# Kernel tuning notes

Measured on AMD Instinct MI355X. Metric: run time of the kernel, lower is better.

The kernel has to match this reference:

```python
import jax, jax.numpy as jnp
import numpy as np

H = 128  # hidden_size
I = 28   # input_size
C = 10   # num_classes


def setup_inputs() -> dict:
    key = jax.random.key(0)
    ks = jax.random.split(key, 11)
    s = 1.0 / np.sqrt(H)  # torch nn.RNN init scale
    return {
        "x": jax.random.normal(ks[0], (8192, 28, I), dtype=jnp.float32),
        "W_ih0": jax.random.uniform(ks[1], (H, I), jnp.float32, -s, s),
        "W_hh0": jax.random.uniform(ks[2], (H, H), jnp.float32, -s, s),
        "b_ih0": jax.random.uniform(ks[3], (H,), jnp.float32, -s, s),
        "b_hh0": jax.random.uniform(ks[4], (H,), jnp.float32, -s, s),
        "W_ih1": jax.random.uniform(ks[5], (H, H), jnp.float32, -s, s),
        "W_hh1": jax.random.uniform(ks[6], (H, H), jnp.float32, -s, s),
        "b_ih1": jax.random.uniform(ks[7], (H,), jnp.float32, -s, s),
        "b_hh1": jax.random.uniform(ks[8], (H,), jnp.float32, -s, s),
        "fc_w": jax.random.uniform(ks[9], (C, H), jnp.float32, -s, s),
        "fc_b": jax.random.uniform(ks[10], (C,), jnp.float32, -s, s),
    }


def _rnn_layer_full(x, W_ih, b_ih, W_hh, b_hh):
    # x: [B, T, D] -> full output sequence [B, T, H]
    B = x.shape[0]
    h0 = jnp.zeros((B, H), x.dtype)
    xw = jnp.einsum('btd,hd->bth', x, W_ih) + b_ih  # precompute input GEMM

    def step(h, xw_t):
        h = jnp.tanh(xw_t + h @ W_hh.T + b_hh)
        return h, h

    _, ys = jax.lax.scan(step, h0, jnp.swapaxes(xw, 0, 1))  # [T, B, H]
    return jnp.swapaxes(ys, 0, 1)


def _rnn_layer_last(x, W_ih, b_ih, W_hh, b_hh):
    # only the final hidden state is needed downstream
    B = x.shape[0]
    h0 = jnp.zeros((B, H), x.dtype)
    xw = jnp.einsum('btd,hd->bth', x, W_ih) + b_ih

    def step(h, xw_t):
        h = jnp.tanh(xw_t + h @ W_hh.T + b_hh)
        return h, None

    h_last, _ = jax.lax.scan(step, h0, jnp.swapaxes(xw, 0, 1))
    return h_last


def reference(x, W_ih0, W_hh0, b_ih0, b_hh0, W_ih1, W_hh1, b_ih1, b_hh1, fc_w, fc_b):
    out0 = _rnn_layer_full(x, W_ih0, b_ih0, W_hh0, b_hh0)   # [B, T, H]
    h_last = _rnn_layer_last(out0, W_ih1, b_ih1, W_hh1, b_hh1)  # [B, H] == out[:, -1, :]
    return h_last @ fc_w.T + fc_b  # [B, C]
```

## Files before the change

### kernel.cpp

```cpp
#include <hip/hip_runtime.h>

#define HSZ 128
#define ISZ 28
#define TSZ 28
#define CSZ 10
#define BT  16
#define NT  256
#define HBUF 2048

typedef _Float16 half_t;
typedef _Float16 v8h __attribute__((ext_vector_type(8)));
typedef _Float16 v4h __attribute__((ext_vector_type(4)));
typedef float v4f __attribute__((ext_vector_type(4)));

__device__ __forceinline__ float fast_tanh(float x) {
    float e = __expf(2.f * x);
    return 1.f - 2.f * __builtin_amdgcn_rcpf(e + 1.f);
}

__global__ __launch_bounds__(NT, 2)
void rnn_mfma6(const float* __restrict__ x,
               const float* __restrict__ W_ih0, const float* __restrict__ W_hh0,
               const float* __restrict__ b_ih0, const float* __restrict__ b_hh0,
               const float* __restrict__ W_ih1, const float* __restrict__ W_hh1,
               const float* __restrict__ b_ih1, const float* __restrict__ b_hh1,
               const float* __restrict__ fc_w, const float* __restrict__ fc_b,
               float* __restrict__ out)
{
    __shared__ half_t h0s[2][HBUF];
    __shared__ half_t h1s[2][HBUF];
    __shared__ half_t xs[TSZ][512];

    const int tid  = threadIdx.x;
    const int wave = tid >> 6;
    const int lane = tid & 63;
    const int ln   = lane & 15;
    const int quad = lane >> 4;
    const int b0   = blockIdx.x * BT;
    const int wbase = wave * 32;

    v8h aWx[2], aW0[2][4], aW1i[2][4], aW1h[2][4];
    v4f bias0[2], bias1[2];
#pragma unroll
    for (int rt = 0; rt < 2; ++rt) {
        const int row = wbase + rt * 16 + ln;
        {
            float4 p = *(const float4*)(b_ih0 + wbase + rt * 16 + quad * 4);
            float4 q = *(const float4*)(b_hh0 + wbase + rt * 16 + quad * 4);
            bias0[rt] = (v4f){p.x + q.x, p.y + q.y, p.z + q.z, p.w + q.w};
            p = *(const float4*)(b_ih1 + wbase + rt * 16 + quad * 4);
            q = *(const float4*)(b_hh1 + wbase + rt * 16 + quad * 4);
            bias1[rt] = (v4f){p.x + q.x, p.y + q.y, p.z + q.z, p.w + q.w};
        }
        {
            const float* pw = W_ih0 + row * ISZ + quad * 8;
            float4 a = *(const float4*)pw;
            float4 b = (quad < 3) ? *(const float4*)(pw + 4) : make_float4(0.f, 0.f, 0.f, 0.f);
            aWx[rt] = (v8h){(half_t)a.x, (half_t)a.y, (half_t)a.z, (half_t)a.w,
                            (half_t)b.x, (half_t)b.y, (half_t)b.z, (half_t)b.w};
        }
#pragma unroll
        for (int ks = 0; ks < 4; ++ks) {
            const float4* p0 = (const float4*)(W_hh0 + row * HSZ + ks * 32 + quad * 8);
            const float4* p1 = (const float4*)(W_ih1 + row * HSZ + ks * 32 + quad * 8);
            const float4* p2 = (const float4*)(W_hh1 + row * HSZ + ks * 32 + quad * 8);
            float4 a = p0[0], b = p0[1];
            aW0[rt][ks] = (v8h){(half_t)a.x, (half_t)a.y, (half_t)a.z, (half_t)a.w,
                                (half_t)b.x, (half_t)b.y, (half_t)b.z, (half_t)b.w};
            a = p1[0]; b = p1[1];
            aW1i[rt][ks] = (v8h){(half_t)a.x, (half_t)a.y, (half_t)a.z, (half_t)a.w,
                                 (half_t)b.x, (half_t)b.y, (half_t)b.z, (half_t)b.w};
            a = p2[0]; b = p2[1];
            aW1h[rt][ks] = (v8h){(half_t)a.x, (half_t)a.y, (half_t)a.z, (half_t)a.w,
                                 (half_t)b.x, (half_t)b.y, (half_t)b.z, (half_t)b.w};
        }
    }

    {
#pragma unroll
        for (int it = 0; it < 7; ++it) {
            const int c = tid + it * NT;
            const int q = c & 3;
            const int n = (c >> 2) & 15;
            const int t = c >> 6;
            const float* g = x + ((size_t)(b0 + n) * TSZ + t) * ISZ + q * 8;
            float4 a = *(const float4*)g;
            float4 b = (q < 3) ? *(const float4*)(g + 4) : make_float4(0.f, 0.f, 0.f, 0.f);
            v8h p = {(half_t)a.x, (half_t)a.y, (half_t)a.z, (half_t)a.w,
                     (half_t)b.x, (half_t)b.y, (half_t)b.z, (half_t)b.w};
            *(v8h*)&xs[t][(q * 16 + n) * 8] = p;
        }
    }

    *(v8h*)&h1s[0][tid * 8] = (v8h){(half_t)0.f, (half_t)0.f, (half_t)0.f, (half_t)0.f,
                                    (half_t)0.f, (half_t)0.f, (half_t)0.f, (half_t)0.f};
    __syncthreads();

    const int ws0 = wave * 512 + (quad >> 1) * 128 + ln * 8 + (quad & 1) * 4;
    const int ws1 = ws0 + 256;
    const int ro = lane * 8;

    {
        const v8h bx = *(const v8h*)&xs[0][ro];
#pragma unroll
        for (int rt = 0; rt < 2; ++rt) {
            v4f c = bias0[rt];
            c = __builtin_amdgcn_mfma_f32_16x16x32_f16(aWx[rt], bx, c, 0, 0, 0);
            v4h p = {(half_t)fast_tanh(c[0]), (half_t)fast_tanh(c[1]),
                     (half_t)fast_tanh(c[2]), (half_t)fast_tanh(c[3])};
            *(v4h*)&h0s[0][rt ? ws1 : ws0] = p;
        }
    }
    __syncthreads();

#pragma unroll 2
    for (int t = 0; t < TSZ - 1; ++t) {
        const int pr = t & 1;

        v8h bh0[4], bh1[4];
#pragma unroll
        for (int ks = 0; ks < 4; ++ks)
            bh0[ks] = *(const v8h*)&h0s[pr][ks * 512 + ro];
        const v8h bx = *(const v8h*)&xs[t + 1][ro];
#pragma unroll
        for (int ks = 0; ks < 4; ++ks)
            bh1[ks] = *(const v8h*)&h1s[pr][ks * 512 + ro];

#pragma unroll
        for (int rt = 0; rt < 2; ++rt) {
            v4f c = bias0[rt];
            c = __builtin_amdgcn_mfma_f32_16x16x32_f16(aWx[rt], bx, c, 0, 0, 0);
#pragma unroll
            for (int ks = 0; ks < 4; ++ks)
                c = __builtin_amdgcn_mfma_f32_16x16x32_f16(aW0[rt][ks], bh0[ks], c, 0, 0, 0);
            v4h p = {(half_t)fast_tanh(c[0]), (half_t)fast_tanh(c[1]),
                     (half_t)fast_tanh(c[2]), (half_t)fast_tanh(c[3])};
            *(v4h*)&h0s[pr ^ 1][rt ? ws1 : ws0] = p;
        }

#pragma unroll
        for (int rt = 0; rt < 2; ++rt) {
            v4f si = bias1[rt];
            v4f sh = (v4f){0.f, 0.f, 0.f, 0.f};
#pragma unroll
            for (int ks = 0; ks < 4; ++ks) {
                si = __builtin_amdgcn_mfma_f32_16x16x32_f16(aW1i[rt][ks], bh0[ks], si, 0, 0, 0);
                sh = __builtin_amdgcn_mfma_f32_16x16x32_f16(aW1h[rt][ks], bh1[ks], sh, 0, 0, 0);
            }
            const v4f a1 = si + sh;
            v4h p = {(half_t)fast_tanh(a1[0]), (half_t)fast_tanh(a1[1]),
                     (half_t)fast_tanh(a1[2]), (half_t)fast_tanh(a1[3])};
            *(v4h*)&h1s[pr ^ 1][rt ? ws1 : ws0] = p;
        }

        __syncthreads();
    }

    {
        const int pr = (TSZ - 1) & 1;
        v8h bh0[4], bh1[4];
#pragma unroll
        for (int ks = 0; ks < 4; ++ks) {
            bh0[ks] = *(const v8h*)&h0s[pr][ks * 512 + ro];
            bh1[ks] = *(const v8h*)&h1s[pr][ks * 512 + ro];
        }
#pragma unroll
        for (int rt = 0; rt < 2; ++rt) {
            v4f si = bias1[rt];
            v4f sh = (v4f){0.f, 0.f, 0.f, 0.f};
#pragma unroll
            for (int ks = 0; ks < 4; ++ks) {
                si = __builtin_amdgcn_mfma_f32_16x16x32_f16(aW1i[rt][ks], bh0[ks], si, 0, 0, 0);
                sh = __builtin_amdgcn_mfma_f32_16x16x32_f16(aW1h[rt][ks], bh1[ks], sh, 0, 0, 0);
            }
            const v4f a1 = si + sh;
            v4h p = {(half_t)fast_tanh(a1[0]), (half_t)fast_tanh(a1[1]),
                     (half_t)fast_tanh(a1[2]), (half_t)fast_tanh(a1[3])};
            *(v4h*)&h1s[pr ^ 1][rt ? ws1 : ws0] = p;
        }
    }
    __syncthreads();

    if (tid < BT * CSZ) {
        const int m = tid / CSZ, cc = tid - m * CSZ;
        float s = fc_b[cc];
#pragma unroll
        for (int ks = 0; ks < 4; ++ks) {
#pragma unroll
            for (int q2 = 0; q2 < 4; ++q2) {
                const v8h hv = *(const v8h*)&h1s[0][(ks * 64 + q2 * 16 + m) * 8];
                const int kb = ks * 32 + q2 * 8;
                const float4 w0 = *(const float4*)(fc_w + cc * HSZ + kb);
                const float4 w1 = *(const float4*)(fc_w + cc * HSZ + kb + 4);
                s += (float)hv[0] * w0.x + (float)hv[1] * w0.y +
                     (float)hv[2] * w0.z + (float)hv[3] * w0.w +
                     (float)hv[4] * w1.x + (float)hv[5] * w1.y +
                     (float)hv[6] * w1.z + (float)hv[7] * w1.w;
            }
        }
        out[(b0 + m) * CSZ + cc] = s;
    }
}

extern "C" void kernel_launch(void* const* d_in, const int* in_sizes, int n_in,
                              void* d_out, int out_size, void* d_ws, size_t ws_size,
                              hipStream_t stream) {
    const float* x     = (const float*)d_in[0];
    const float* W_ih0 = (const float*)d_in[1];
    const float* W_hh0 = (const float*)d_in[2];
    const float* b_ih0 = (const float*)d_in[3];
    const float* b_hh0 = (const float*)d_in[4];
    const float* W_ih1 = (const float*)d_in[5];
    const float* W_hh1 = (const float*)d_in[6];
    const float* b_ih1 = (const float*)d_in[7];
    const float* b_hh1 = (const float*)d_in[8];
    const float* fc_w  = (const float*)d_in[9];
    const float* fc_b  = (const float*)d_in[10];
    float* out = (float*)d_out;

    const int B = in_sizes[0] / (TSZ * ISZ);
    dim3 grid(B / BT), block(NT);
    rnn_mfma6<<<grid, block, 0, stream>>>(x, W_ih0, W_hh0, b_ih0, b_hh0,
                                          W_ih1, W_hh1, b_ih1, b_hh1,
                                          fc_w, fc_b, out);
}
```

Measured before the change: 128.1 us.

## Split layers into producer/consumer wave groups with flag-based ring-buffer sync

Four waves now run only the layer-0 recurrence and four waves run only the layer-1 recurrence. They hand hidden states through a 4-slot LDS ring and signal progress with per-wave volatile flags in shared memory, replacing the per-step block barrier. Each block now handles 32 sequences in two groups of 16 with 512 threads. This lets layer 0 run up to three steps ahead of layer 1, so the two layers overlap and register pressure per wave drops. It adds spin-wait polling on LDS and relies on LDS memory-ordering assumptions (waitcnt before the flag write) for correctness.

```diff
diff --git a/kernel.cpp b/kernel.cpp
--- a/kernel.cpp
+++ b/kernel.cpp
@@ -4,9 +4,9 @@
 #define ISZ 28
 #define TSZ 28
 #define CSZ 10
-#define BT  16
-#define NT  256
-#define HBUF 2048
+#define BT  32
+#define NG  2
+#define NT  512
 
 typedef _Float16 half_t;
 typedef _Float16 v8h __attribute__((ext_vector_type(8)));
@@ -18,18 +18,21 @@
     return 1.f - 2.f * __builtin_amdgcn_rcpf(e + 1.f);
 }
 
+__device__ __forceinline__ int imin(int a, int b) { return a < b ? a : b; }
+
 __global__ __launch_bounds__(NT, 2)
-void rnn_mfma6(const float* __restrict__ x,
-               const float* __restrict__ W_ih0, const float* __restrict__ W_hh0,
-               const float* __restrict__ b_ih0, const float* __restrict__ b_hh0,
-               const float* __restrict__ W_ih1, const float* __restrict__ W_hh1,
-               const float* __restrict__ b_ih1, const float* __restrict__ b_hh1,
-               const float* __restrict__ fc_w, const float* __restrict__ fc_b,
-               float* __restrict__ out)
+void rnn_pc(const float* __restrict__ x,
+            const float* __restrict__ W_ih0, const float* __restrict__ W_hh0,
+            const float* __restrict__ b_ih0, const float* __restrict__ b_hh0,
+            const float* __restrict__ W_ih1, const float* __restrict__ W_hh1,
+            const float* __restrict__ b_ih1, const float* __restrict__ b_hh1,
+            const float* __restrict__ fc_w, const float* __restrict__ fc_b,
+            float* __restrict__ out)
 {
-    __shared__ half_t h0s[2][HBUF];
-    __shared__ half_t h1s[2][HBUF];
-    __shared__ half_t xs[TSZ][512];
+    __shared__ half_t h0r[4][NG][2048];
+    __shared__ half_t h1r[4][NG][2048];
+    __shared__ half_t xs[TSZ][NG][512];
+    __shared__ int    flags[8];
 
     const int tid  = threadIdx.x;
     const int wave = tid >> 6;
@@ -37,158 +40,157 @@
     const int ln   = lane & 15;
     const int quad = lane >> 4;
     const int b0   = blockIdx.x * BT;
-    const int wbase = wave * 32;
-
-    v8h aWx[2], aW0[2][4], aW1i[2][4], aW1h[2][4];
-    v4f bias0[2], bias1[2];
-#pragma unroll
-    for (int rt = 0; rt < 2; ++rt) {
-        const int row = wbase + rt * 16 + ln;
-        {
-            float4 p = *(const float4*)(b_ih0 + wbase + rt * 16 + quad * 4);
-            float4 q = *(const float4*)(b_hh0 + wbase + rt * 16 + quad * 4);
+    const int w4   = wave & 3;
+    const int wsl  = w4 * 512 + (quad >> 1) * 128 + ln * 8 + (quad & 1) * 4;
+    const int ro   = lane * 8;
+    volatile int* vf = (volatile int*)flags;
+
+    {
+#pragma unroll
+        for (int it = 0; it < 7; ++it) {
+            const int c = tid + it * NT;
+            const int q = c & 3;
+            const int n = (c >> 2) & 15;
+            const int g = (c >> 6) & 1;
+            const int t = c >> 7;
+            const float* gp = x + ((size_t)(b0 + g * 16 + n) * TSZ + t) * ISZ + q * 8;
+            float4 a = *(const float4*)gp;
+            float4 b = (q < 3) ? *(const float4*)(gp + 4) : make_float4(0.f, 0.f, 0.f, 0.f);
+            v8h p = {(half_t)a.x, (half_t)a.y, (half_t)a.z, (half_t)a.w,
+                     (half_t)b.x, (half_t)b.y, (half_t)b.z, (half_t)b.w};
+            *(v8h*)&xs[t][g][(q * 16 + n) * 8] = p;
+        }
+    }
+    {
+        const v8h z = {(half_t)0.f, (half_t)0.f, (half_t)0.f, (half_t)0.f,
+                       (half_t)0.f, (half_t)0.f, (half_t)0.f, (half_t)0.f};
+        *(v8h*)&h0r[3][0][tid * 8] = z;
+        *(v8h*)&h1r[3][0][tid * 8] = z;
+        if (tid < 8) flags[tid] = 0;
+    }
+    __syncthreads();
+
+    if (wave < 4) {
+        v8h aWx[2], aW0[2][4];
+        v4f bias0[2];
+#pragma unroll
+        for (int rt = 0; rt < 2; ++rt) {
+            const int row = w4 * 32 + rt * 16 + ln;
+            float4 p = *(const float4*)(b_ih0 + w4 * 32 + rt * 16 + quad * 4);
+            float4 q = *(const float4*)(b_hh0 + w4 * 32 + rt * 16 + quad * 4);
             bias0[rt] = (v4f){p.x + q.x, p.y + q.y, p.z + q.z, p.w + q.w};
-            p = *(const float4*)(b_ih1 + wbase + rt * 16 + quad * 4);
-            q = *(const float4*)(b_hh1 + wbase + rt * 16 + quad * 4);
-            bias1[rt] = (v4f){p.x + q.x, p.y + q.y, p.z + q.z, p.w + q.w};
-        }
-        {
             const float* pw = W_ih0 + row * ISZ + quad * 8;
             float4 a = *(const float4*)pw;
             float4 b = (quad < 3) ? *(const float4*)(pw + 4) : make_float4(0.f, 0.f, 0.f, 0.f);
             aWx[rt] = (v8h){(half_t)a.x, (half_t)a.y, (half_t)a.z, (half_t)a.w,
                             (half_t)b.x, (half_t)b.y, (half_t)b.z, (half_t)b.w};
-        }
-#pragma unroll
-        for (int ks = 0; ks < 4; ++ks) {
-            const float4* p0 = (const float4*)(W_hh0 + row * HSZ + ks * 32 + quad * 8);
-            const float4* p1 = (const float4*)(W_ih1 + row * HSZ + ks * 32 + quad * 8);
-            const float4* p2 = (const float4*)(W_hh1 + row * HSZ + ks * 32 + quad * 8);
-            float4 a = p0[0], b = p0[1];
-            aW0[rt][ks] = (v8h){(half_t)a.x, (half_t)a.y, (half_t)a.z, (half_t)a.w,
-                                (half_t)b.x, (half_t)b.y, (half_t)b.z, (half_t)b.w};
-            a = p1[0]; b = p1[1];
-            aW1i[rt][ks] = (v8h){(half_t)a.x, (half_t)a.y, (half_t)a.z, (half_t)a.w,
-                                 (half_t)b.x, (half_t)b.y, (half_t)b.z, (half_t)b.w};
-            a = p2[0]; b = p2[1];
-            aW1h[rt][ks] = (v8h){(half_t)a.x, (half_t)a.y, (half_t)a.z, (half_t)a.w,
-                                 (half_t)b.x, (half_t)b.y, (half_t)b.z, (half_t)b.w};
-        }
-    }
-
-    {
-#pragma unroll
-        for (int it = 0; it < 7; ++it) {
-            const int c = tid + it * NT;
-            const int q = c & 3;
-            const int n = (c >> 2) & 15;
-            const int t = c >> 6;
-            const float* g = x + ((size_t)(b0 + n) * TSZ + t) * ISZ + q * 8;
-            float4 a = *(const float4*)g;
-            float4 b = (q < 3) ? *(const float4*)(g + 4) : make_float4(0.f, 0.f, 0.f, 0.f);
-            v8h p = {(half_t)a.x, (half_t)a.y, (half_t)a.z, (half_t)a.w,
-                     (half_t)b.x, (half_t)b.y, (half_t)b.z, (half_t)b.w};
-            *(v8h*)&xs[t][(q * 16 + n) * 8] = p;
-        }
-    }
-
-    *(v8h*)&h1s[0][tid * 8] = (v8h){(half_t)0.f, (half_t)0.f, (half_t)0.f, (half_t)0.f,
-                                    (half_t)0.f, (half_t)0.f, (half_t)0.f, (half_t)0.f};
-    __syncthreads();
-
-    const int ws0 = wave * 512 + (quad >> 1) * 128 + ln * 8 + (quad & 1) * 4;
-    const int ws1 = ws0 + 256;
-    const int ro = lane * 8;
-
-    {
-        const v8h bx = *(const v8h*)&xs[0][ro];
+#pragma unroll
+            for (int ks = 0; ks < 4; ++ks) {
+                const float4* p0 = (const float4*)(W_hh0 + row * HSZ + ks * 32 + quad * 8);
+                float4 c = p0[0], d = p0[1];
+                aW0[rt][ks] = (v8h){(half_t)c.x, (half_t)c.y, (half_t)c.z, (half_t)c.w,
+                                    (half_t)d.x, (half_t)d.y, (half_t)d.z, (half_t)d.w};
+            }
+        }
+
+        for (int t = 0; t < TSZ; ++t) {
+            for (;;) {
+                int m0 = imin(imin(vf[0], vf[1]), imin(vf[2], vf[3]));
+                int m1 = imin(imin(vf[4], vf[5]), imin(vf[6], vf[7]));
+                if (m0 >= t && m1 >= t - 3) break;
+            }
+            __asm__ volatile("" ::: "memory");
+            const int sr = (t + 3) & 3, sw = t & 3;
+#pragma unroll
+            for (int g = 0; g < NG; ++g) {
+                v8h bh[4];
+#pragma unroll
+                for (int ks = 0; ks < 4; ++ks)
+                    bh[ks] = *(const v8h*)&h0r[sr][g][ks * 512 + ro];
+                const v8h bx = *(const v8h*)&xs[t][g][ro];
+#pragma unroll
+                for (int rt = 0; rt < 2; ++rt) {
+                    v4f c = bias0[rt];
+                    c = __builtin_amdgcn_mfma_f32_16x16x32_f16(aWx[rt], bx, c, 0, 0, 0);
+#pragma unroll
+                    for (int ks = 0; ks < 4; ++ks)
+                        c = __builtin_amdgcn_mfma_f32_16x16x32_f16(aW0[rt][ks], bh[ks], c, 0, 0, 0);
+                    v4h p = {(half_t)fast_tanh(c[0]), (half_t)fast_tanh(c[1]),
+                             (half_t)fast_tanh(c[2]), (half_t)fast_tanh(c[3])};
+                    *(v4h*)&h0r[sw][g][wsl + rt * 256] = p;
+                }
+            }
+            __asm__ volatile("s_waitcnt lgkmcnt(0)" ::: "memory");
+            if (lane == 0) vf[w4] = t + 1;
+        }
+    } else {
+        v8h aW1i[2][4], aW1h[2][4];
+        v4f bias1[2];
 #pragma unroll
         for (int rt = 0; rt < 2; ++rt) {
-            v4f c = bias0[rt];
-            c = __builtin_amdgcn_mfma_f32_16x16x32_f16(aWx[rt], bx, c, 0, 0, 0);
-            v4h p = {(half_t)fast_tanh(c[0]), (half_t)fast_tanh(c[1]),
-                     (half_t)fast_tanh(c[2]), (half_t)fast_tanh(c[3])};
-            *(v4h*)&h0s[0][rt ? ws1 : ws0] = p;
-        }
-    }
-    __syncthreads();
-
-#pragma unroll 2
-    for (int t = 0; t < TSZ - 1; ++t) {
-        const int pr = t & 1;
-
-        v8h bh0[4], bh1[4];
-#pragma unroll
-        for (int ks = 0; ks < 4; ++ks)
-            bh0[ks] = *(const v8h*)&h0s[pr][ks * 512 + ro];
-        const v8h bx = *(const v8h*)&xs[t + 1][ro];
-#pragma unroll
-        for (int ks = 0; ks < 4; ++ks)
-            bh1[ks] = *(const v8h*)&h1s[pr][ks * 512 + ro];
-
-#pragma unroll
-        for (int rt = 0; rt < 2; ++rt) {
-            v4f c = bias0[rt];
-            c = __builtin_amdgcn_mfma_f32_16x16x32_f16(aWx[rt], bx, c, 0, 0, 0);
-#pragma unroll
-            for (int ks = 0; ks < 4; ++ks)
-                c = __builtin_amdgcn_mfma_f32_16x16x32_f16(aW0[rt][ks], bh0[ks], c, 0, 0, 0);
-            v4h p = {(half_t)fast_tanh(c[0]), (half_t)fast_tanh(c[1]),
-                     (half_t)fast_tanh(c[2]), (half_t)fast_tanh(c[3])};
-            *(v4h*)&h0s[pr ^ 1][rt ? ws1 : ws0] = p;
-        }
-
-#pragma unroll
-        for (int rt = 0; rt < 2; ++rt) {
-            v4f si = bias1[rt];
-            v4f sh = (v4f){0.f, 0.f, 0.f, 0.f};
+            const int row = w4 * 32 + rt * 16 + ln;
+            float4 p = *(const float4*)(b_ih1 + w4 * 32 + rt * 16 + quad * 4);
+            float4 q = *(const float4*)(b_hh1 + w4 * 32 + rt * 16 + quad * 4);
+            bias1[rt] = (v4f){p.x + q.x, p.y + q.y, p.z + q.z, p.w + q.w};
 #pragma unroll
             for (int ks = 0; ks < 4; ++ks) {
-                si = __builtin_amdgcn_mfma_f32_16x16x32_f16(aW1i[rt][ks], bh0[ks], si, 0, 0, 0);
-                sh = __builtin_amdgcn_mfma_f32_16x16x32_f16(aW1h[rt][ks], bh1[ks], sh, 0, 0, 0);
-            }
-            const v4f a1 = si + sh;
-            v4h p = {(half_t)fast_tanh(a1[0]), (half_t)fast_tanh(a1[1]),
-                     (half_t)fast_tanh(a1[2]), (half_t)fast_tanh(a1[3])};
-            *(v4h*)&h1s[pr ^ 1][rt ? ws1 : ws0] = p;
-        }
-
-        __syncthreads();
-    }
-
-    {
-        const int pr = (TSZ - 1) & 1;
-        v8h bh0[4], bh1[4];
-#pragma unroll
-        for (int ks = 0; ks < 4; ++ks) {
-            bh0[ks] = *(const v8h*)&h0s[pr][ks * 512 + ro];
-            bh1[ks] = *(const v8h*)&h1s[pr][ks * 512 + ro];
-        }
-#pragma unroll
-        for (int rt = 0; rt < 2; ++rt) {
-            v4f si = bias1[rt];
-            v4f sh = (v4f){0.f, 0.f, 0.f, 0.f};
-#pragma unroll
-            for (int ks = 0; ks < 4; ++ks) {
-                si = __builtin_amdgcn_mfma_f32_16x16x32_f16(aW1i[rt][ks], bh0[ks], si, 0, 0, 0);
-                sh = __builtin_amdgcn_mfma_f32_16x16x32_f16(aW1h[rt][ks], bh1[ks], sh, 0, 0, 0);
-            }
-            const v4f a1 = si + sh;
-            v4h p = {(half_t)fast_tanh(a1[0]), (half_t)fast_tanh(a1[1]),
-                     (half_t)fast_tanh(a1[2]), (half_t)fast_tanh(a1[3])};
-            *(v4h*)&h1s[pr ^ 1][rt ? ws1 : ws0] = p;
+                const float4* p1 = (const float4*)(W_ih1 + row * HSZ + ks * 32 + quad * 8);
+                const float4* p2 = (const float4*)(W_hh1 + row * HSZ + ks * 32 + quad * 8);
+                float4 a = p1[0], b = p1[1];
+                aW1i[rt][ks] = (v8h){(half_t)a.x, (half_t)a.y, (half_t)a.z, (half_t)a.w,
+                                     (half_t)b.x, (half_t)b.y, (half_t)b.z, (half_t)b.w};
+                a = p2[0]; b = p2[1];
+                aW1h[rt][ks] = (v8h){(half_t)a.x, (half_t)a.y, (half_t)a.z, (half_t)a.w,
+                                     (half_t)b.x, (half_t)b.y, (half_t)b.z, (half_t)b.w};
+            }
+        }
+
+        for (int t = 0; t < TSZ; ++t) {
+            for (;;) {
+                int m0 = imin(imin(vf[0], vf[1]), imin(vf[2], vf[3]));
+                int m1 = imin(imin(vf[4], vf[5]), imin(vf[6], vf[7]));
+                if (m0 >= t + 1 && m1 >= t) break;
+            }
+            __asm__ volatile("" ::: "memory");
+            const int s0 = t & 3, s1 = (t + 3) & 3;
+#pragma unroll
+            for (int g = 0; g < NG; ++g) {
+                v8h bh0[4], bh1[4];
+#pragma unroll
+                for (int ks = 0; ks < 4; ++ks) {
+                    bh0[ks] = *(const v8h*)&h0r[s0][g][ks * 512 + ro];
+                    bh1[ks] = *(const v8h*)&h1r[s1][g][ks * 512 + ro];
+                }
+#pragma unroll
+                for (int rt = 0; rt < 2; ++rt) {
+                    v4f si = bias1[rt];
+                    v4f sh = (v4f){0.f, 0.f, 0.f, 0.f};
+#pragma unroll
+                    for (int ks = 0; ks < 4; ++ks) {
+                        si = __builtin_amdgcn_mfma_f32_16x16x32_f16(aW1i[rt][ks], bh0[ks], si, 0, 0, 0);
+                        sh = __builtin_amdgcn_mfma_f32_16x16x32_f16(aW1h[rt][ks], bh1[ks], sh, 0, 0, 0);
+                    }
+                    const v4f a1 = si + sh;
+                    v4h p = {(half_t)fast_tanh(a1[0]), (half_t)fast_tanh(a1[1]),
+                             (half_t)fast_tanh(a1[2]), (half_t)fast_tanh(a1[3])};
+                    *(v4h*)&h1r[s0][g][wsl + rt * 256] = p;
+                }
+            }
+            __asm__ volatile("s_waitcnt lgkmcnt(0)" ::: "memory");
+            if (lane == 0) vf[4 + w4] = t + 1;
         }
     }
     __syncthreads();
 
     if (tid < BT * CSZ) {
         const int m = tid / CSZ, cc = tid - m * CSZ;
+        const int g = m >> 4, n = m & 15;
         float s = fc_b[cc];
 #pragma unroll
         for (int ks = 0; ks < 4; ++ks) {
 #pragma unroll
             for (int q2 = 0; q2 < 4; ++q2) {
-                const v8h hv = *(const v8h*)&h1s[0][(ks * 64 + q2 * 16 + m) * 8];
+                const v8h hv = *(const v8h*)&h1r[3][g][(ks * 64 + q2 * 16 + n) * 8];
                 const int kb = ks * 32 + q2 * 8;
                 const float4 w0 = *(const float4*)(fc_w + cc * HSZ + kb);
                 const float4 w1 = *(const float4*)(fc_w + cc * HSZ + kb + 4);
@@ -220,7 +222,7 @@
 
     const int B = in_sizes[0] / (TSZ * ISZ);
     dim3 grid(B / BT), block(NT);
-    rnn_mfma6<<<grid, block, 0, stream>>>(x, W_ih0, W_hh0, b_ih0, b_hh0,
-                                          W_ih1, W_hh1, b_ih1, b_hh1,
-                                          fc_w, fc_b, out);
+    rnn_pc<<<grid, block, 0, stream>>>(x, W_ih0, W_hh0, b_ih0, b_hh0,
+                                       W_ih1, W_hh1, b_ih1, b_hh1,
+                                       fc_w, fc_b, out);
 }
```

Measured after the change: 131.6 us. 2.7% more time.
